# Kernel optimization log

Hardware: AMD Instinct MI355X
Metric: run time of the kernel (lower is better)

The kernel has to match this reference:

```python
import jax, jax.numpy as jnp
import numpy as np

B, S, D, E, L = 4, 384, 300, 50, 2
HD = D // L  # head_dim = 150


def _linear_params(k, fin, fout):
    bnd = 1.0 / np.sqrt(fin)
    kw, kb = jax.random.split(k)
    W = jax.random.uniform(kw, (fout, fin), minval=-bnd, maxval=bnd, dtype=jnp.float32)
    b = jax.random.uniform(kb, (fout,), minval=-bnd, maxval=bnd, dtype=jnp.float32)
    return W, b


def setup_inputs() -> dict:
    key = jax.random.key(0)
    ks = jax.random.split(key, 6)
    W0, b0 = _linear_params(ks[0], D, HD)            # weight_list[0]: Linear(300, 150)
    W1, b1 = _linear_params(ks[1], D + HD, HD)       # weight_list[1]: Linear(450, 150)
    Wh, bh = _linear_params(ks[2], 2 * HD + E, E)    # Edgeupdate.W: Linear(350, 50)
    Wout, bout = _linear_params(ks[3], D, D)         # linear_output: Linear(300, 300)
    adj = jax.random.uniform(ks[4], (B, S, S, E), dtype=jnp.float32)
    gcn_inputs = jax.random.normal(ks[5], (B, S, D), dtype=jnp.float32)
    return dict(adj=adj, gcn_inputs=gcn_inputs, W0=W0, b0=b0, W1=W1, b1=b1,
                Wh=Wh, bh=bh, Wout=Wout, bout=bout)


def reference(adj, gcn_inputs, W0, b0, W1, b1, Wh, bh, Wout, bout):
    # Edgeupdate weight split: cat order is [edge(E), node1(HD), node2(HD)]
    Wh_e = Wh[:, :E]            # [E, E]
    Wh_1 = Wh[:, E:E + HD]      # [E, HD]
    Wh_2 = Wh[:, E + HD:]       # [E, HD]

    outputs = gcn_inputs        # [B, S, D]
    cache = [gcn_inputs]
    out_list = []
    for (Wl, bl) in ((W0, b0), (W1, b1)):
        e_dim = adj.shape[-1]
        # mean over edge channels of (adj_e @ outputs): einsum fuses the mean
        Ax = jnp.einsum('bike,bkd->bid', adj, outputs) / e_dim   # [B, S, din]
        # AxW = W_l(Ax) + W_l(outputs)  (same linear applied twice, bias twice)
        AxW = (Ax @ Wl.T + bl) + (outputs @ Wl.T + bl)           # [B, S, HD]
        gAxW = jax.nn.relu(AxW)
        # Edgeupdate highway: new_edge[b,i,j] = W([edge[b,i,j]; g[b,j]; g[b,i]]) + bh
        # (node1[b,i,j] = g[b,j], node2[b,i,j] = g[b,i] from the expand/permute)
        edge_part = adj @ Wh_e.T                                  # [B, S, S, E]
        n1 = gAxW @ Wh_1.T                                        # [B, S, E]
        n2 = gAxW @ Wh_2.T                                        # [B, S, E]
        adj = edge_part + n1[:, None, :, :] + n2[:, :, None, :] + bh
        cache.append(gAxW)
        outputs = jnp.concatenate(cache, axis=2)                  # growing concat
        out_list.append(gAxW)  # gcn_drop is identity in eval mode

    gcn_outputs = jnp.concatenate(out_list, axis=2) + gcn_inputs  # [B, S, D]
    return gcn_outputs @ Wout.T + bout
```

## Files before the change

kernel.cpp:

```cpp
#include <hip/hip_runtime.h>

constexpr int Bc  = 4;
constexpr int Sc  = 384;
constexpr int Dc  = 300;
constexpr int Ec  = 50;
constexpr int HDc = 150;
constexpr int WHC = 350;

typedef __attribute__((ext_vector_type(8))) short bf16x8;
typedef __attribute__((ext_vector_type(4))) float f32x4;

__device__ __forceinline__ short f2bf(float x) {
    union { float f; unsigned u; } v; v.f = x;
    unsigned r = (v.u + 0x7FFFu + ((v.u >> 16) & 1u)) >> 16;
    return (short)r;
}

__global__ void prep_kernel(const float* __restrict__ Wh,
                            const float* __restrict__ bh,
                            float* __restrict__ sm) {
    int t = threadIdx.x;
    if (t < Ec) {
        float s = 0.f;
        for (int e = 0; e < Ec; ++e) s += Wh[e*WHC + t];
        sm[t] = s;
    } else if (t >= 64 && t < 64 + HDc) {
        int h = t - 64;
        float s = 0.f;
        for (int e = 0; e < Ec; ++e) s += Wh[e*WHC + Ec + h];
        sm[t] = s;
    } else if (t >= 224 && t < 224 + HDc) {
        int h = t - 224;
        float s = 0.f;
        for (int e = 0; e < Ec; ++e) s += Wh[e*WHC + Ec + HDc + h];
        sm[t] = s;
    } else if (t == 384) {
        float s = 0.f;
        for (int e = 0; e < Ec; ++e) s += bh[e];
        sm[t] = s;
    }
}

__global__ __launch_bounds__(256)
void reduce_adj3(const float* __restrict__ adj, const float* __restrict__ sm,
                 float* __restrict__ A0, float* __restrict__ wadj) {
    __shared__ float tile[64 * 51];
    __shared__ float wec[64];
    int t = threadIdx.x;
    if (t < Ec) wec[t] = sm[t];

    long base = (long)blockIdx.x * 3200;
    const float4* p4 = (const float4*)(adj + base);
    float4 v0 = p4[t];
    float4 v1 = p4[t + 256];
    float4 v2 = p4[t + 512];
    float4 v3 = {0.f, 0.f, 0.f, 0.f};
    if (t < 32) v3 = p4[t + 768];

    auto scat = [&](int i, const float4& v) {
        const float* vp = (const float*)&v;
        #pragma unroll
        for (int j = 0; j < 4; ++j) {
            int e = 4 * i + j;
            tile[(e / 50) * 51 + (e % 50)] = vp[j];
        }
    };
    scat(t, v0);
    scat(t + 256, v1);
    scat(t + 512, v2);
    if (t < 32) scat(t + 768, v3);
    __syncthreads();

    int r = t >> 2, q = t & 3;
    int h0 = q * 13, h1 = (q == 3) ? 50 : h0 + 13;
    const float* row = tile + r * 51;
    float s = 0.f, w = 0.f;
    for (int i = h0; i < h1; ++i) { float v = row[i]; s += v; w += v * wec[i]; }
    s += __shfl_xor(s, 1); w += __shfl_xor(w, 1);
    s += __shfl_xor(s, 2); w += __shfl_xor(w, 2);
    if (q == 0) {
        int g = blockIdx.x * 64 + r;
        A0[g]   = s * (1.0f / Ec);
        wadj[g] = w;
    }
}

template<int BSRC, int A1M, int HASD, int HASB, int RELU>
__global__ __launch_bounds__(256)
void mgemm(const float* __restrict__ A, int lda, long sA,
           const float* __restrict__ Bw, int ldb, long sB,
           const float* __restrict__ W1a, const float* __restrict__ WoutP,
           const float* __restrict__ Dm, int ldd, long sD,
           const float* __restrict__ bias, float bscale,
           const float* __restrict__ s12, const float* __restrict__ sm,
           float* __restrict__ C, int ldc, long sC,
           int M, int N, int K)
{
    const int b = blockIdx.z;
    const float* Ap = A + (long)b * sA;
    const float* Bp = Bw + (long)b * sB;
    const float* Dp = Dm + (long)b * sD;
    float* Cp = C + (long)b * sC;

    __shared__ short As[32 * 72];
    __shared__ short Bs[32 * 72];

    const int tid  = threadIdx.x;
    const int wave = tid >> 6, lane = tid & 63;
    const int wm = wave & 1, wn = wave >> 1;
    const int lm = lane & 15, quad = lane >> 4;
    const int m0 = blockIdx.y * 32, n0 = blockIdx.x * 32;

    const int srow = tid >> 3;
    const int sk   = (tid & 7) * 8;
    const int nc   = tid & 31;
    const int kr   = tid >> 5;

    float sbh = 0.f; const float* s1p = nullptr; float s2v = 0.f;
    if constexpr (A1M) {
        sbh = sm[384];
        s1p = s12 + 2L * Sc * b;
        s2v = s1p[2 * (m0 + srow) + 1];
    }

    float ra[8], rb[8];

    auto stageA = [&](int k0) {
        int am = m0 + srow;
        int kb = k0 + sk;
        if constexpr (A1M) {
            float4 u = *(const float4*)(Ap + (long)am * lda + kb);
            float4 w = *(const float4*)(Ap + (long)am * lda + kb + 4);
            const float* up = (const float*)&u;
            const float* wp = (const float*)&w;
            #pragma unroll
            for (int j = 0; j < 4; ++j) {
                ra[j]     = (up[j] + s1p[2*(kb + j)]     + s2v + sbh) * (1.0f/Ec);
                ra[4 + j] = (wp[j] + s1p[2*(kb + 4 + j)] + s2v + sbh) * (1.0f/Ec);
            }
        } else {
            if (kb + 7 < K) {
                float4 u = *(const float4*)(Ap + (long)am * lda + kb);
                float4 w = *(const float4*)(Ap + (long)am * lda + kb + 4);
                ra[0]=u.x; ra[1]=u.y; ra[2]=u.z; ra[3]=u.w;
                ra[4]=w.x; ra[5]=w.y; ra[6]=w.z; ra[7]=w.w;
            } else {
                #pragma unroll
                for (int j = 0; j < 8; ++j) {
                    int k = kb + j;
                    ra[j] = (k < K) ? Ap[(long)am * lda + k] : 0.f;
                }
            }
        }
    };

    auto stageB = [&](int k0) {
        if constexpr (BSRC == 0) {
            int n = n0 + nc;
            bool nok = n < N;
            #pragma unroll
            for (int p = 0; p < 8; ++p) {
                int k = k0 + kr + p * 8;
                rb[p] = nok ? Bp[(long)k * ldb + n] : 0.f;
            }
        } else {
            int nr = n0 + srow;
            bool nok = nr < N;
            const float* wp = Bp; int ld = ldb; int nn = nr;
            if constexpr (BSRC == 2) {
                if (nr < 150)      { wp = Bp;    ld = 300; nn = nr; }
                else if (nr < 300) { wp = W1a;   ld = 450; nn = nr - 150; }
                else               { wp = WoutP; ld = 300; nn = nr - 300; }
            }
            #pragma unroll
            for (int p = 0; p < 4; ++p) {
                int k = k0 + sk + 2 * p;
                if (nok && k + 1 < K) {
                    float2 v = *(const float2*)(wp + (long)nn * ld + k);
                    rb[2*p] = v.x; rb[2*p + 1] = v.y;
                } else {
                    rb[2*p]     = (nok && k < K)     ? wp[(long)nn * ld + k]     : 0.f;
                    rb[2*p + 1] = (nok && k + 1 < K) ? wp[(long)nn * ld + k + 1] : 0.f;
                }
            }
        }
    };

    auto stash = [&]() {
        #pragma unroll
        for (int j = 0; j < 8; ++j) As[srow * 72 + sk + j] = f2bf(ra[j]);
        if constexpr (BSRC == 0) {
            #pragma unroll
            for (int p = 0; p < 8; ++p) Bs[nc * 72 + kr + p * 8] = f2bf(rb[p]);
        } else {
            #pragma unroll
            for (int j = 0; j < 8; ++j) Bs[srow * 72 + sk + j] = f2bf(rb[j]);
        }
    };

    f32x4 acc = {0.f, 0.f, 0.f, 0.f};

    stageA(0); stageB(0);
    for (int k0 = 0; k0 < K; k0 += 64) {
        __syncthreads();
        stash();
        __syncthreads();
        if (k0 + 64 < K) { stageA(k0 + 64); stageB(k0 + 64); }
        {
            bf16x8 a0 = *(const bf16x8*)(As + (wm*16 + lm) * 72 + quad * 8);
            bf16x8 b0 = *(const bf16x8*)(Bs + (wn*16 + lm) * 72 + quad * 8);
            acc = __builtin_amdgcn_mfma_f32_16x16x32_bf16(a0, b0, acc, 0, 0, 0);
            bf16x8 a1 = *(const bf16x8*)(As + (wm*16 + lm) * 72 + 32 + quad * 8);
            bf16x8 b1 = *(const bf16x8*)(Bs + (wn*16 + lm) * 72 + 32 + quad * 8);
            acc = __builtin_amdgcn_mfma_f32_16x16x32_bf16(a1, b1, acc, 0, 0, 0);
        }
    }

    int cn = n0 + wn * 16 + lm;
    if (cn < N) {
        #pragma unroll
        for (int r = 0; r < 4; ++r) {
            int cm = m0 + wm * 16 + quad * 4 + r;
            if (cm < M) {
                float v = acc[r];
                if constexpr (HASD) v += Dp[(long)cm * ldd + cn];
                if constexpr (HASB) v += bscale * bias[cn];
                if constexpr (RELU) v = fmaxf(v, 0.f);
                Cp[(long)cm * ldc + cn] = v;
            }
        }
    }
}

__global__ __launch_bounds__(256)
void s12k(const float* __restrict__ G, const float* __restrict__ sm,
          float* __restrict__ s12) {
    int wave = threadIdx.x >> 6, lane = threadIdx.x & 63;
    int g = blockIdx.x * 4 + wave;
    const float* gp = G + (long)g * Dc;
    float a = 0.f, c = 0.f;
    #pragma unroll
    for (int h0 = 0; h0 < HDc; h0 += 64) {
        int h = h0 + lane;
        if (h < HDc) { float v = gp[h]; a += v * sm[64 + h]; c += v * sm[224 + h]; }
    }
    #pragma unroll
    for (int off = 32; off; off >>= 1) {
        a += __shfl_down(a, off);
        c += __shfl_down(c, off);
    }
    if (lane == 0) { s12[2*g] = a; s12[2*g + 1] = c; }
}

extern "C" void kernel_launch(void* const* d_in, const int* in_sizes, int n_in,
                              void* d_out, int out_size, void* d_ws, size_t ws_size,
                              hipStream_t stream) {
    const float* adj  = (const float*)d_in[0];
    const float* X    = (const float*)d_in[1];
    const float* W0   = (const float*)d_in[2];
    const float* b0   = (const float*)d_in[3];
    const float* W1   = (const float*)d_in[4];
    const float* b1   = (const float*)d_in[5];
    const float* Wh   = (const float*)d_in[6];
    const float* bh   = (const float*)d_in[7];
    const float* Wout = (const float*)d_in[8];
    const float* bout = (const float*)d_in[9];
    float* out = (float*)d_out;

    float* ws   = (float*)d_ws;
    float* sm   = ws;
    float* A0   = sm + 512;
    float* wadj = A0 + Bc * Sc * Sc;
    float* R    = wadj + Bc * Sc * Sc;
    float* Gbuf = R + (long)Bc * Sc * 600;
    float* s12  = Gbuf + (long)Bc * Sc * Dc;

    const int MT = Bc * Sc;
    const long AS = (long)Sc * Sc;
    const long RS = (long)Sc * 600;
    const long GS = (long)Sc * Dc;

    prep_kernel<<<1, 512, 0, stream>>>(Wh, bh, sm);

    reduce_adj3<<<(Bc*Sc*Sc) / 64, 256, 0, stream>>>(adj, sm, A0, wadj);

    mgemm<2,0,0,0,0><<<dim3(19, 48, 1), 256, 0, stream>>>(
        X, Dc, 0, W0, 300, 0, W1, Wout,
        nullptr, 0, 0, nullptr, 0.f, nullptr, nullptr,
        R, 600, 0, MT, 600, Dc);

    mgemm<0,0,1,1,1><<<dim3(5, 12, Bc), 256, 0, stream>>>(
        A0, Sc, AS, R, 600, RS, nullptr, nullptr,
        R, 600, RS, b0, 2.0f, nullptr, nullptr,
        Gbuf, Dc, GS, Sc, HDc, Sc);

    s12k<<<MT / 4, 256, 0, stream>>>(Gbuf, sm, s12);

    mgemm<1,0,1,0,0><<<dim3(5, 48, 1), 256, 0, stream>>>(
        Gbuf, Dc, 0, W1 + Dc, Dc + HDc, 0, nullptr, nullptr,
        R + HDc, 600, 0, nullptr, 0.f, nullptr, nullptr,
        R + HDc, 600, 0, MT, HDc, HDc);

    mgemm<0,1,1,1,1><<<dim3(5, 12, Bc), 256, 0, stream>>>(
        wadj, Sc, AS, R + HDc, 600, RS, nullptr, nullptr,
        R + HDc, 600, RS, b1, 2.0f, s12, sm,
        Gbuf + HDc, Dc, GS, Sc, HDc, Sc);

    mgemm<1,0,1,1,0><<<dim3(10, 48, 1), 256, 0, stream>>>(
        Gbuf, Dc, 0, Wout, Dc, 0, nullptr, nullptr,
        R + 2*HDc, 600, 0, bout, 1.0f, nullptr, nullptr,
        out, Dc, 0, MT, Dc, Dc);
}
```

Measured before the change: 242.9 us.

## Fuse all stages into one cooperative persistent kernel with grid syncs

```diff
diff --git a/kernel.cpp b/kernel.cpp
--- a/kernel.cpp
+++ b/kernel.cpp
@@ -1,4 +1,7 @@
 #include <hip/hip_runtime.h>
+#include <hip/hip_cooperative_groups.h>
+
+namespace cg = cooperative_groups;
 
 constexpr int Bc  = 4;
 constexpr int Sc  = 384;
@@ -6,6 +9,7 @@
 constexpr int Ec  = 50;
 constexpr int HDc = 150;
 constexpr int WHC = 350;
+constexpr int MT  = Bc * Sc;
 
 typedef __attribute__((ext_vector_type(8))) short bf16x8;
 typedef __attribute__((ext_vector_type(4))) float f32x4;
@@ -14,6 +18,334 @@
     union { float f; unsigned u; } v; v.f = x;
     unsigned r = (v.u + 0x7FFFu + ((v.u >> 16) & 1u)) >> 16;
     return (short)r;
+}
+
+
+__device__ __forceinline__ void reduce_unit(
+    float* tile, const float* wec,
+    const float* __restrict__ adj,
+    float* __restrict__ A0, float* __restrict__ wadj, int unit)
+{
+    int t = threadIdx.x;
+    __syncthreads();
+    long base = (long)unit * 3200;
+    const float4* p4 = (const float4*)(adj + base);
+    float4 v0 = p4[t];
+    float4 v1 = p4[t + 256];
+    float4 v2 = p4[t + 512];
+    float4 v3 = {0.f, 0.f, 0.f, 0.f};
+    if (t < 32) v3 = p4[t + 768];
+
+    auto scat = [&](int i, const float4& v) {
+        const float* vp = (const float*)&v;
+        #pragma unroll
+        for (int j = 0; j < 4; ++j) {
+            int e = 4 * i + j;
+            tile[(e / 50) * 51 + (e % 50)] = vp[j];
+        }
+    };
+    scat(t, v0);
+    scat(t + 256, v1);
+    scat(t + 512, v2);
+    if (t < 32) scat(t + 768, v3);
+    __syncthreads();
+
+    int r = t >> 2, q = t & 3;
+    int h0 = q * 13, h1 = (q == 3) ? 50 : h0 + 13;
+    const float* row = tile + r * 51;
+    float s = 0.f, w = 0.f;
+    for (int i = h0; i < h1; ++i) { float v = row[i]; s += v; w += v * wec[i]; }
+    s += __shfl_xor(s, 1); w += __shfl_xor(w, 1);
+    s += __shfl_xor(s, 2); w += __shfl_xor(w, 2);
+    if (q == 0) {
+        int g = unit * 64 + r;
+        A0[g]   = s * (1.0f / Ec);
+        wadj[g] = w;
+    }
+}
+
+__device__ __forceinline__ void s12_unit(const float* __restrict__ G,
+                                         const float* __restrict__ sm,
+                                         float* __restrict__ s12, int unit)
+{
+    int wave = threadIdx.x >> 6, lane = threadIdx.x & 63;
+    int g = unit * 4 + wave;
+    const float* gp = G + (long)g * Dc;
+    float a = 0.f, c = 0.f;
+    #pragma unroll
+    for (int h0 = 0; h0 < HDc; h0 += 64) {
+        int h = h0 + lane;
+        if (h < HDc) { float v = gp[h]; a += v * sm[64 + h]; c += v * sm[224 + h]; }
+    }
+    #pragma unroll
+    for (int off = 32; off; off >>= 1) {
+        a += __shfl_down(a, off);
+        c += __shfl_down(c, off);
+    }
+    if (lane == 0) { s12[2*g] = a; s12[2*g + 1] = c; }
+}
+
+template<int BSRC, int A1M, int HASD, int HASB, int RELU>
+__device__ __forceinline__ void mgemm_body(
+    short* As, short* Bs, int bx, int by, int b,
+    const float* __restrict__ A, int lda, long sA,
+    const float* __restrict__ Bw, int ldb, long sB,
+    const float* __restrict__ W1a, const float* __restrict__ WoutP,
+    const float* __restrict__ Dm, int ldd, long sD,
+    const float* __restrict__ bias, float bscale,
+    const float* __restrict__ s12, const float* __restrict__ sm,
+    float* __restrict__ C, int ldc, long sC,
+    int M, int N, int K)
+{
+    const float* Ap = A + (long)b * sA;
+    const float* Bp = Bw + (long)b * sB;
+    const float* Dp = Dm + (long)b * sD;
+    float* Cp = C + (long)b * sC;
+
+    const int tid  = threadIdx.x;
+    const int wave = tid >> 6, lane = tid & 63;
+    const int wm = wave & 1, wn = wave >> 1;
+    const int lm = lane & 15, quad = lane >> 4;
+    const int m0 = by * 32, n0 = bx * 32;
+
+    const int srow = tid >> 3;
+    const int sk   = (tid & 7) * 8;
+    const int nc   = tid & 31;
+    const int kr   = tid >> 5;
+
+    float sbh = 0.f; const float* s1p = nullptr; float s2v = 0.f;
+    if constexpr (A1M) {
+        sbh = sm[384];
+        s1p = s12 + 2L * Sc * b;
+        s2v = s1p[2 * (m0 + srow) + 1];
+    }
+
+    float ra[8], rb[8];
+
+    auto stageA = [&](int k0) {
+        int am = m0 + srow;
+        int kb = k0 + sk;
+        if constexpr (A1M) {
+            float4 u = *(const float4*)(Ap + (long)am * lda + kb);
+            float4 w = *(const float4*)(Ap + (long)am * lda + kb + 4);
+            const float* up = (const float*)&u;
+            const float* wp = (const float*)&w;
+            #pragma unroll
+            for (int j = 0; j < 4; ++j) {
+                ra[j]     = (up[j] + s1p[2*(kb + j)]     + s2v + sbh) * (1.0f/Ec);
+                ra[4 + j] = (wp[j] + s1p[2*(kb + 4 + j)] + s2v + sbh) * (1.0f/Ec);
+            }
+        } else {
+            if (kb + 7 < K) {
+                float4 u = *(const float4*)(Ap + (long)am * lda + kb);
+                float4 w = *(const float4*)(Ap + (long)am * lda + kb + 4);
+                ra[0]=u.x; ra[1]=u.y; ra[2]=u.z; ra[3]=u.w;
+                ra[4]=w.x; ra[5]=w.y; ra[6]=w.z; ra[7]=w.w;
+            } else {
+                #pragma unroll
+                for (int j = 0; j < 8; ++j) {
+                    int k = kb + j;
+                    ra[j] = (k < K) ? Ap[(long)am * lda + k] : 0.f;
+                }
+            }
+        }
+    };
+
+    auto stageB = [&](int k0) {
+        if constexpr (BSRC == 0) {
+            int n = n0 + nc;
+            bool nok = n < N;
+            #pragma unroll
+            for (int p = 0; p < 8; ++p) {
+                int k = k0 + kr + p * 8;
+                rb[p] = nok ? Bp[(long)k * ldb + n] : 0.f;
+            }
+        } else {
+            int nr = n0 + srow;
+            bool nok = nr < N;
+            const float* wp = Bp; int ld = ldb; int nn = nr;
+            if constexpr (BSRC == 2) {
+                if (nr < 150)      { wp = Bp;    ld = 300; nn = nr; }
+                else if (nr < 300) { wp = W1a;   ld = 450; nn = nr - 150; }
+                else               { wp = WoutP; ld = 300; nn = nr - 300; }
+            }
+            #pragma unroll
+            for (int p = 0; p < 4; ++p) {
+                int k = k0 + sk + 2 * p;
+                if (nok && k + 1 < K) {
+                    float2 v = *(const float2*)(wp + (long)nn * ld + k);
+                    rb[2*p] = v.x; rb[2*p + 1] = v.y;
+                } else {
+                    rb[2*p]     = (nok && k < K)     ? wp[(long)nn * ld + k]     : 0.f;
+                    rb[2*p + 1] = (nok && k + 1 < K) ? wp[(long)nn * ld + k + 1] : 0.f;
+                }
+            }
+        }
+    };
+
+    auto stash = [&]() {
+        #pragma unroll
+        for (int j = 0; j < 8; ++j) As[srow * 72 + sk + j] = f2bf(ra[j]);
+        if constexpr (BSRC == 0) {
+            #pragma unroll
+            for (int p = 0; p < 8; ++p) Bs[nc * 72 + kr + p * 8] = f2bf(rb[p]);
+        } else {
+            #pragma unroll
+            for (int j = 0; j < 8; ++j) Bs[srow * 72 + sk + j] = f2bf(rb[j]);
+        }
+    };
+
+    f32x4 acc = {0.f, 0.f, 0.f, 0.f};
+
+    stageA(0); stageB(0);
+    for (int k0 = 0; k0 < K; k0 += 64) {
+        __syncthreads();
+        stash();
+        __syncthreads();
+        if (k0 + 64 < K) { stageA(k0 + 64); stageB(k0 + 64); }
+        {
+            bf16x8 a0 = *(const bf16x8*)(As + (wm*16 + lm) * 72 + quad * 8);
+            bf16x8 b0 = *(const bf16x8*)(Bs + (wn*16 + lm) * 72 + quad * 8);
+            acc = __builtin_amdgcn_mfma_f32_16x16x32_bf16(a0, b0, acc, 0, 0, 0);
+            bf16x8 a1 = *(const bf16x8*)(As + (wm*16 + lm) * 72 + 32 + quad * 8);
+            bf16x8 b1 = *(const bf16x8*)(Bs + (wn*16 + lm) * 72 + 32 + quad * 8);
+            acc = __builtin_amdgcn_mfma_f32_16x16x32_bf16(a1, b1, acc, 0, 0, 0);
+        }
+    }
+
+    int cn = n0 + wn * 16 + lm;
+    if (cn < N) {
+        #pragma unroll
+        for (int r = 0; r < 4; ++r) {
+            int cm = m0 + wm * 16 + quad * 4 + r;
+            if (cm < M) {
+                float v = acc[r];
+                if constexpr (HASD) v += Dp[(long)cm * ldd + cn];
+                if constexpr (HASB) v += bscale * bias[cn];
+                if constexpr (RELU) v = fmaxf(v, 0.f);
+                Cp[(long)cm * ldc + cn] = v;
+            }
+        }
+    }
+}
+
+__global__ __launch_bounds__(256, 4)
+void mega(const float* __restrict__ adj, const float* __restrict__ X,
+          const float* __restrict__ W0, const float* __restrict__ b0,
+          const float* __restrict__ W1, const float* __restrict__ b1,
+          const float* __restrict__ Wh, const float* __restrict__ bh,
+          const float* __restrict__ Wout, const float* __restrict__ bout,
+          float* __restrict__ sm, float* __restrict__ A0,
+          float* __restrict__ wadj, float* __restrict__ R,
+          float* __restrict__ Gbuf, float* __restrict__ s12,
+          float* __restrict__ out)
+{
+    __shared__ float ldsf[64 * 51 + 64];
+    short* As   = (short*)ldsf;
+    short* Bs   = As + 32 * 72;
+    float* tile = ldsf;
+    float* wec  = ldsf + 64 * 51;
+
+    const int bid = blockIdx.x, nb = gridDim.x;
+    const int t = threadIdx.x;
+
+    if (t < Ec) {
+        float s = 0.f;
+        for (int e = 0; e < Ec; ++e) s += Wh[e * WHC + t];
+        wec[t] = s;
+    }
+    if (bid == 0) {
+        for (int u = t; u < 512; u += 256) {
+            if (u < Ec) {
+                float s = 0.f;
+                for (int e = 0; e < Ec; ++e) s += Wh[e*WHC + u];
+                sm[u] = s;
+            } else if (u >= 64 && u < 64 + HDc) {
+                int h = u - 64; float s = 0.f;
+                for (int e = 0; e < Ec; ++e) s += Wh[e*WHC + Ec + h];
+                sm[u] = s;
+            } else if (u >= 224 && u < 224 + HDc) {
+                int h = u - 224; float s = 0.f;
+                for (int e = 0; e < Ec; ++e) s += Wh[e*WHC + Ec + HDc + h];
+                sm[u] = s;
+            } else if (u == 384) {
+                float s = 0.f;
+                for (int e = 0; e < Ec; ++e) s += bh[e];
+                sm[u] = s;
+            }
+        }
+    }
+    __syncthreads();
+
+    const long AS = (long)Sc * Sc;
+    const long RS = (long)Sc * 600;
+    const long GS = (long)Sc * Dc;
+
+    cg::grid_group grid = cg::this_grid();
+
+    {
+        const int UR = (Bc * Sc * Sc) / 64;
+        const int UT = UR + 19 * 48;
+        for (int u = bid; u < UT; u += nb) {
+            if (u < UR) {
+                reduce_unit(tile, wec, adj, A0, wadj, u);
+            } else {
+                int v = u - UR;
+                mgemm_body<2,0,0,0,0>(As, Bs, v % 19, v / 19, 0,
+                    X, Dc, 0, W0, 300, 0, W1, Wout,
+                    nullptr, 0, 0, nullptr, 0.f, nullptr, nullptr,
+                    R, 600, 0, MT, 600, Dc);
+            }
+        }
+    }
+    grid.sync();
+
+    for (int u = bid; u < 5 * 12 * Bc; u += nb) {
+        mgemm_body<0,0,1,1,1>(As, Bs, u % 5, (u / 5) % 12, u / 60,
+            A0, Sc, AS, R, 600, RS, nullptr, nullptr,
+            R, 600, RS, b0, 2.0f, nullptr, nullptr,
+            Gbuf, Dc, GS, Sc, HDc, Sc);
+    }
+    grid.sync();
+
+    {
+        const int U1 = MT / 4;
+        const int U2 = U1 + 5 * 48;
+        const int U3 = U2 + 10 * 48;
+        for (int u = bid; u < U3; u += nb) {
+            if (u < U1) {
+                s12_unit(Gbuf, sm, s12, u);
+            } else if (u < U2) {
+                int v = u - U1;
+                mgemm_body<1,0,1,0,0>(As, Bs, v % 5, v / 5, 0,
+                    Gbuf, Dc, 0, W1 + Dc, Dc + HDc, 0, nullptr, nullptr,
+                    R + HDc, 600, 0, nullptr, 0.f, nullptr, nullptr,
+                    R + HDc, 600, 0, MT, HDc, HDc);
+            } else {
+                int v = u - U2;
+                mgemm_body<1,0,1,1,0>(As, Bs, v % 10, v / 10, 0,
+                    Gbuf, Dc, 0, Wout, Dc, 0, nullptr, nullptr,
+                    R + 2 * HDc, 600, 0, bout, 1.0f, nullptr, nullptr,
+                    out, Dc, 0, MT, Dc, HDc);
+            }
+        }
+    }
+    grid.sync();
+
+    for (int u = bid; u < 5 * 12 * Bc; u += nb) {
+        mgemm_body<0,1,1,1,1>(As, Bs, u % 5, (u / 5) % 12, u / 60,
+            wadj, Sc, AS, R + HDc, 600, RS, nullptr, nullptr,
+            R + HDc, 600, RS, b1, 2.0f, s12, sm,
+            Gbuf + HDc, Dc, GS, Sc, HDc, Sc);
+    }
+    grid.sync();
+
+    for (int u = bid; u < 10 * 48; u += nb) {
+        mgemm_body<1,0,1,0,0>(As, Bs, u % 10, u / 10, 0,
+            Gbuf + HDc, Dc, 0, Wout + HDc, Dc, 0, nullptr, nullptr,
+            out, Dc, 0, nullptr, 0.f, nullptr, nullptr,
+            out, Dc, 0, MT, Dc, HDc);
+    }
 }
 
 __global__ void prep_kernel(const float* __restrict__ Wh,
@@ -44,45 +376,11 @@
 __global__ __launch_bounds__(256)
 void reduce_adj3(const float* __restrict__ adj, const float* __restrict__ sm,
                  float* __restrict__ A0, float* __restrict__ wadj) {
-    __shared__ float tile[64 * 51];
-    __shared__ float wec[64];
-    int t = threadIdx.x;
-    if (t < Ec) wec[t] = sm[t];
-
-    long base = (long)blockIdx.x * 3200;
-    const float4* p4 = (const float4*)(adj + base);
-    float4 v0 = p4[t];
-    float4 v1 = p4[t + 256];
-    float4 v2 = p4[t + 512];
-    float4 v3 = {0.f, 0.f, 0.f, 0.f};
-    if (t < 32) v3 = p4[t + 768];
-
-    auto scat = [&](int i, const float4& v) {
-        const float* vp = (const float*)&v;
-        #pragma unroll
-        for (int j = 0; j < 4; ++j) {
-            int e = 4 * i + j;
-            tile[(e / 50) * 51 + (e % 50)] = vp[j];
-        }
-    };
-    scat(t, v0);
-    scat(t + 256, v1);
-    scat(t + 512, v2);
-    if (t < 32) scat(t + 768, v3);
-    __syncthreads();
-
-    int r = t >> 2, q = t & 3;
-    int h0 = q * 13, h1 = (q == 3) ? 50 : h0 + 13;
-    const float* row = tile + r * 51;
-    float s = 0.f, w = 0.f;
-    for (int i = h0; i < h1; ++i) { float v = row[i]; s += v; w += v * wec[i]; }
-    s += __shfl_xor(s, 1); w += __shfl_xor(w, 1);
-    s += __shfl_xor(s, 2); w += __shfl_xor(w, 2);
-    if (q == 0) {
-        int g = blockIdx.x * 64 + r;
-        A0[g]   = s * (1.0f / Ec);
-        wadj[g] = w;
-    }
+    __shared__ float lds[64 * 51 + 64];
+    float* tile = lds;
+    float* wec  = lds + 64 * 51;
+    if (threadIdx.x < Ec) wec[threadIdx.x] = sm[threadIdx.x];
+    reduce_unit(tile, wec, adj, A0, wadj, blockIdx.x);
 }
 
 template<int BSRC, int A1M, int HASD, int HASB, int RELU>
@@ -96,160 +394,18 @@
            float* __restrict__ C, int ldc, long sC,
            int M, int N, int K)
 {
-    const int b = blockIdx.z;
-    const float* Ap = A + (long)b * sA;
-    const float* Bp = Bw + (long)b * sB;
-    const float* Dp = Dm + (long)b * sD;
-    float* Cp = C + (long)b * sC;
-
     __shared__ short As[32 * 72];
     __shared__ short Bs[32 * 72];
-
-    const int tid  = threadIdx.x;
-    const int wave = tid >> 6, lane = tid & 63;
-    const int wm = wave & 1, wn = wave >> 1;
-    const int lm = lane & 15, quad = lane >> 4;
-    const int m0 = blockIdx.y * 32, n0 = blockIdx.x * 32;
-
-    const int srow = tid >> 3;
-    const int sk   = (tid & 7) * 8;
-    const int nc   = tid & 31;
-    const int kr   = tid >> 5;
-
-    float sbh = 0.f; const float* s1p = nullptr; float s2v = 0.f;
-    if constexpr (A1M) {
-        sbh = sm[384];
-        s1p = s12 + 2L * Sc * b;
-        s2v = s1p[2 * (m0 + srow) + 1];
-    }
-
-    float ra[8], rb[8];
-
-    auto stageA = [&](int k0) {
-        int am = m0 + srow;
-        int kb = k0 + sk;
-        if constexpr (A1M) {
-            float4 u = *(const float4*)(Ap + (long)am * lda + kb);
-            float4 w = *(const float4*)(Ap + (long)am * lda + kb + 4);
-            const float* up = (const float*)&u;
-            const float* wp = (const float*)&w;
-            #pragma unroll
-            for (int j = 0; j < 4; ++j) {
-                ra[j]     = (up[j] + s1p[2*(kb + j)]     + s2v + sbh) * (1.0f/Ec);
-                ra[4 + j] = (wp[j] + s1p[2*(kb + 4 + j)] + s2v + sbh) * (1.0f/Ec);
-            }
-        } else {
-            if (kb + 7 < K) {
-                float4 u = *(const float4*)(Ap + (long)am * lda + kb);
-                float4 w = *(const float4*)(Ap + (long)am * lda + kb + 4);
-                ra[0]=u.x; ra[1]=u.y; ra[2]=u.z; ra[3]=u.w;
-                ra[4]=w.x; ra[5]=w.y; ra[6]=w.z; ra[7]=w.w;
-            } else {
-                #pragma unroll
-                for (int j = 0; j < 8; ++j) {
-                    int k = kb + j;
-                    ra[j] = (k < K) ? Ap[(long)am * lda + k] : 0.f;
-                }
-            }
-        }
-    };
-
-    auto stageB = [&](int k0) {
-        if constexpr (BSRC == 0) {
-            int n = n0 + nc;
-            bool nok = n < N;
-            #pragma unroll
-            for (int p = 0; p < 8; ++p) {
-                int k = k0 + kr + p * 8;
-                rb[p] = nok ? Bp[(long)k * ldb + n] : 0.f;
-            }
-        } else {
-            int nr = n0 + srow;
-            bool nok = nr < N;
-            const float* wp = Bp; int ld = ldb; int nn = nr;
-            if constexpr (BSRC == 2) {
-                if (nr < 150)      { wp = Bp;    ld = 300; nn = nr; }
-                else if (nr < 300) { wp = W1a;   ld = 450; nn = nr - 150; }
-                else               { wp = WoutP; ld = 300; nn = nr - 300; }
-            }
-            #pragma unroll
-            for (int p = 0; p < 4; ++p) {
-                int k = k0 + sk + 2 * p;
-                if (nok && k + 1 < K) {
-                    float2 v = *(const float2*)(wp + (long)nn * ld + k);
-                    rb[2*p] = v.x; rb[2*p + 1] = v.y;
-                } else {
-                    rb[2*p]     = (nok && k < K)     ? wp[(long)nn * ld + k]     : 0.f;
-                    rb[2*p + 1] = (nok && k + 1 < K) ? wp[(long)nn * ld + k + 1] : 0.f;
-                }
-            }
-        }
-    };
-
-    auto stash = [&]() {
-        #pragma unroll
-        for (int j = 0; j < 8; ++j) As[srow * 72 + sk + j] = f2bf(ra[j]);
-        if constexpr (BSRC == 0) {
-            #pragma unroll
-            for (int p = 0; p < 8; ++p) Bs[nc * 72 + kr + p * 8] = f2bf(rb[p]);
-        } else {
-            #pragma unroll
-            for (int j = 0; j < 8; ++j) Bs[srow * 72 + sk + j] = f2bf(rb[j]);
-        }
-    };
-
-    f32x4 acc = {0.f, 0.f, 0.f, 0.f};
-
-    stageA(0); stageB(0);
-    for (int k0 = 0; k0 < K; k0 += 64) {
-        __syncthreads();
-        stash();
-        __syncthreads();
-        if (k0 + 64 < K) { stageA(k0 + 64); stageB(k0 + 64); }
-        {
-            bf16x8 a0 = *(const bf16x8*)(As + (wm*16 + lm) * 72 + quad * 8);
-            bf16x8 b0 = *(const bf16x8*)(Bs + (wn*16 + lm) * 72 + quad * 8);
-            acc = __builtin_amdgcn_mfma_f32_16x16x32_bf16(a0, b0, acc, 0, 0, 0);
-            bf16x8 a1 = *(const bf16x8*)(As + (wm*16 + lm) * 72 + 32 + quad * 8);
-            bf16x8 b1 = *(const bf16x8*)(Bs + (wn*16 + lm) * 72 + 32 + quad * 8);
-            acc = __builtin_amdgcn_mfma_f32_16x16x32_bf16(a1, b1, acc, 0, 0, 0);
-        }
-    }
-
-    int cn = n0 + wn * 16 + lm;
-    if (cn < N) {
-        #pragma unroll
-        for (int r = 0; r < 4; ++r) {
-            int cm = m0 + wm * 16 + quad * 4 + r;
-            if (cm < M) {
-                float v = acc[r];
-                if constexpr (HASD) v += Dp[(long)cm * ldd + cn];
-                if constexpr (HASB) v += bscale * bias[cn];
-                if constexpr (RELU) v = fmaxf(v, 0.f);
-                Cp[(long)cm * ldc + cn] = v;
-            }
-        }
-    }
+    mgemm_body<BSRC,A1M,HASD,HASB,RELU>(As, Bs,
+        blockIdx.x, blockIdx.y, blockIdx.z,
+        A, lda, sA, Bw, ldb, sB, W1a, WoutP, Dm, ldd, sD,
+        bias, bscale, s12, sm, C, ldc, sC, M, N, K);
 }
 
 __global__ __launch_bounds__(256)
 void s12k(const float* __restrict__ G, const float* __restrict__ sm,
           float* __restrict__ s12) {
-    int wave = threadIdx.x >> 6, lane = threadIdx.x & 63;
-    int g = blockIdx.x * 4 + wave;
-    const float* gp = G + (long)g * Dc;
-    float a = 0.f, c = 0.f;
-    #pragma unroll
-    for (int h0 = 0; h0 < HDc; h0 += 64) {
-        int h = h0 + lane;
-        if (h < HDc) { float v = gp[h]; a += v * sm[64 + h]; c += v * sm[224 + h]; }
-    }
-    #pragma unroll
-    for (int off = 32; off; off >>= 1) {
-        a += __shfl_down(a, off);
-        c += __shfl_down(c, off);
-    }
-    if (lane == 0) { s12[2*g] = a; s12[2*g + 1] = c; }
+    s12_unit(G, sm, s12, blockIdx.x);
 }
 
 extern "C" void kernel_launch(void* const* d_in, const int* in_sizes, int n_in,
@@ -275,39 +431,60 @@
     float* Gbuf = R + (long)Bc * Sc * 600;
     float* s12  = Gbuf + (long)Bc * Sc * Dc;
 
-    const int MT = Bc * Sc;
     const long AS = (long)Sc * Sc;
     const long RS = (long)Sc * 600;
     const long GS = (long)Sc * Dc;
 
-    prep_kernel<<<1, 512, 0, stream>>>(Wh, bh, sm);
-
-    reduce_adj3<<<(Bc*Sc*Sc) / 64, 256, 0, stream>>>(adj, sm, A0, wadj);
-
-    mgemm<2,0,0,0,0><<<dim3(19, 48, 1), 256, 0, stream>>>(
-        X, Dc, 0, W0, 300, 0, W1, Wout,
-        nullptr, 0, 0, nullptr, 0.f, nullptr, nullptr,
-        R, 600, 0, MT, 600, Dc);
-
-    mgemm<0,0,1,1,1><<<dim3(5, 12, Bc), 256, 0, stream>>>(
-        A0, Sc, AS, R, 600, RS, nullptr, nullptr,
-        R, 600, RS, b0, 2.0f, nullptr, nullptr,
-        Gbuf, Dc, GS, Sc, HDc, Sc);
-
-    s12k<<<MT / 4, 256, 0, stream>>>(Gbuf, sm, s12);
-
-    mgemm<1,0,1,0,0><<<dim3(5, 48, 1), 256, 0, stream>>>(
-        Gbuf, Dc, 0, W1 + Dc, Dc + HDc, 0, nullptr, nullptr,
-        R + HDc, 600, 0, nullptr, 0.f, nullptr, nullptr,
-        R + HDc, 600, 0, MT, HDc, HDc);
-
-    mgemm<0,1,1,1,1><<<dim3(5, 12, Bc), 256, 0, stream>>>(
-        wadj, Sc, AS, R + HDc, 600, RS, nullptr, nullptr,
-        R + HDc, 600, RS, b1, 2.0f, s12, sm,
-        Gbuf + HDc, Dc, GS, Sc, HDc, Sc);
-
-    mgemm<1,0,1,1,0><<<dim3(10, 48, 1), 256, 0, stream>>>(
-        Gbuf, Dc, 0, Wout, Dc, 0, nullptr, nullptr,
-        R + 2*HDc, 600, 0, bout, 1.0f, nullptr, nullptr,
-        out, Dc, 0, MT, Dc, Dc);
-}
+    static int grid_size = 0;
+    if (grid_size == 0) {
+        int nbm = 0;
+        if (hipOccupancyMaxActiveBlocksPerMultiprocessor(&nbm, mega, 256, 0) != hipSuccess || nbm < 1)
+            nbm = 2;
+        int ncu = 256;
+        hipDeviceProp_t prop;
+        int dev = 0;
+        (void)hipGetDevice(&dev);
+        if (hipGetDeviceProperties(&prop, dev) == hipSuccess && prop.multiProcessorCount > 0)
+            ncu = prop.multiProcessorCount;
+        long g = (long)nbm * ncu;
+        if (g > 1024) g = 1024;
+        if (g < 256)  g = 256;
+        grid_size = (int)g;
+    }
+
+    void* args[] = {
+        (void*)&adj, (void*)&X, (void*)&W0, (void*)&b0, (void*)&W1, (void*)&b1,
+        (void*)&Wh, (void*)&bh, (void*)&Wout, (void*)&bout,
+        (void*)&sm, (void*)&A0, (void*)&wadj, (void*)&R, (void*)&Gbuf,
+        (void*)&s12, (void*)&out
+    };
+
+    hipError_t err = hipLaunchCooperativeKernel(mega, dim3(grid_size), dim3(256),
+                                                args, 0u, stream);
+    if (err != hipSuccess) {
+        const int MT_ = MT;
+        prep_kernel<<<1, 512, 0, stream>>>(Wh, bh, sm);
+        reduce_adj3<<<(Bc*Sc*Sc) / 64, 256, 0, stream>>>(adj, sm, A0, wadj);
+        mgemm<2,0,0,0,0><<<dim3(19, 48, 1), 256, 0, stream>>>(
+            X, Dc, 0, W0, 300, 0, W1, Wout,
+            nullptr, 0, 0, nullptr, 0.f, nullptr, nullptr,
+            R, 600, 0, MT_, 600, Dc);
+        mgemm<0,0,1,1,1><<<dim3(5, 12, Bc), 256, 0, stream>>>(
+            A0, Sc, AS, R, 600, RS, nullptr, nullptr,
+            R, 600, RS, b0, 2.0f, nullptr, nullptr,
+            Gbuf, Dc, GS, Sc, HDc, Sc);
+        s12k<<<MT_ / 4, 256, 0, stream>>>(Gbuf, sm, s12);
+        mgemm<1,0,1,0,0><<<dim3(5, 48, 1), 256, 0, stream>>>(
+            Gbuf, Dc, 0, W1 + Dc, Dc + HDc, 0, nullptr, nullptr,
+            R + HDc, 600, 0, nullptr, 0.f, nullptr, nullptr,
+            R + HDc, 600, 0, MT_, HDc, HDc);
+        mgemm<0,1,1,1,1><<<dim3(5, 12, Bc), 256, 0, stream>>>(
+            wadj, Sc, AS, R + HDc, 600, RS, nullptr, nullptr,
+            R + HDc, 600, RS, b1, 2.0f, s12, sm,
+            Gbuf + HDc, Dc, GS, Sc, HDc, Sc);
+        mgemm<1,0,1,1,0><<<dim3(10, 48, 1), 256, 0, stream>>>(
+            Gbuf, Dc, 0, Wout, Dc, 0, nullptr, nullptr,
+            R + 2*HDc, 600, 0, bout, 1.0f, nullptr, nullptr,
+            out, Dc, 0, MT_, Dc, Dc);
+    }
+}
```

Result: slower. 492.0 us (+102.6%).

## Fuse independent kernels into combined launches and split output GEMM by K halves

Applied to the files above, without the earlier changes.

```diff
diff --git a/kernel.cpp b/kernel.cpp
--- a/kernel.cpp
+++ b/kernel.cpp
@@ -6,6 +6,7 @@
 constexpr int Ec  = 50;
 constexpr int HDc = 150;
 constexpr int WHC = 350;
+constexpr int MT  = Bc * Sc;
 
 typedef __attribute__((ext_vector_type(8))) short bf16x8;
 typedef __attribute__((ext_vector_type(4))) float f32x4;
@@ -16,100 +17,49 @@
     return (short)r;
 }
 
-__global__ void prep_kernel(const float* __restrict__ Wh,
-                            const float* __restrict__ bh,
-                            float* __restrict__ sm) {
-    int t = threadIdx.x;
-    if (t < Ec) {
-        float s = 0.f;
-        for (int e = 0; e < Ec; ++e) s += Wh[e*WHC + t];
-        sm[t] = s;
-    } else if (t >= 64 && t < 64 + HDc) {
-        int h = t - 64;
-        float s = 0.f;
-        for (int e = 0; e < Ec; ++e) s += Wh[e*WHC + Ec + h];
-        sm[t] = s;
-    } else if (t >= 224 && t < 224 + HDc) {
-        int h = t - 224;
-        float s = 0.f;
-        for (int e = 0; e < Ec; ++e) s += Wh[e*WHC + Ec + HDc + h];
-        sm[t] = s;
-    } else if (t == 384) {
-        float s = 0.f;
-        for (int e = 0; e < Ec; ++e) s += bh[e];
-        sm[t] = s;
-    }
-}
-
-__global__ __launch_bounds__(256)
-void reduce_adj3(const float* __restrict__ adj, const float* __restrict__ sm,
-                 float* __restrict__ A0, float* __restrict__ wadj) {
-    __shared__ float tile[64 * 51];
-    __shared__ float wec[64];
-    int t = threadIdx.x;
-    if (t < Ec) wec[t] = sm[t];
-
-    long base = (long)blockIdx.x * 3200;
-    const float4* p4 = (const float4*)(adj + base);
-    float4 v0 = p4[t];
-    float4 v1 = p4[t + 256];
-    float4 v2 = p4[t + 512];
-    float4 v3 = {0.f, 0.f, 0.f, 0.f};
-    if (t < 32) v3 = p4[t + 768];
-
-    auto scat = [&](int i, const float4& v) {
-        const float* vp = (const float*)&v;
-        #pragma unroll
-        for (int j = 0; j < 4; ++j) {
-            int e = 4 * i + j;
-            tile[(e / 50) * 51 + (e % 50)] = vp[j];
-        }
-    };
-    scat(t, v0);
-    scat(t + 256, v1);
-    scat(t + 512, v2);
-    if (t < 32) scat(t + 768, v3);
-    __syncthreads();
-
-    int r = t >> 2, q = t & 3;
-    int h0 = q * 13, h1 = (q == 3) ? 50 : h0 + 13;
-    const float* row = tile + r * 51;
-    float s = 0.f, w = 0.f;
-    for (int i = h0; i < h1; ++i) { float v = row[i]; s += v; w += v * wec[i]; }
-    s += __shfl_xor(s, 1); w += __shfl_xor(w, 1);
-    s += __shfl_xor(s, 2); w += __shfl_xor(w, 2);
-    if (q == 0) {
-        int g = blockIdx.x * 64 + r;
-        A0[g]   = s * (1.0f / Ec);
-        wadj[g] = w;
-    }
+__device__ __forceinline__ void s12_unit(const float* __restrict__ G,
+                                         const float* __restrict__ sm,
+                                         float* __restrict__ s12, int unit)
+{
+    int wave = threadIdx.x >> 6, lane = threadIdx.x & 63;
+    int g = unit * 4 + wave;
+    const float* gp = G + (long)g * Dc;
+    float a = 0.f, c = 0.f;
+    #pragma unroll
+    for (int h0 = 0; h0 < HDc; h0 += 64) {
+        int h = h0 + lane;
+        if (h < HDc) { float v = gp[h]; a += v * sm[64 + h]; c += v * sm[224 + h]; }
+    }
+    #pragma unroll
+    for (int off = 32; off; off >>= 1) {
+        a += __shfl_down(a, off);
+        c += __shfl_down(c, off);
+    }
+    if (lane == 0) { s12[2*g] = a; s12[2*g + 1] = c; }
 }
 
 template<int BSRC, int A1M, int HASD, int HASB, int RELU>
-__global__ __launch_bounds__(256)
-void mgemm(const float* __restrict__ A, int lda, long sA,
-           const float* __restrict__ Bw, int ldb, long sB,
-           const float* __restrict__ W1a, const float* __restrict__ WoutP,
-           const float* __restrict__ Dm, int ldd, long sD,
-           const float* __restrict__ bias, float bscale,
-           const float* __restrict__ s12, const float* __restrict__ sm,
-           float* __restrict__ C, int ldc, long sC,
-           int M, int N, int K)
-{
-    const int b = blockIdx.z;
+__device__ __forceinline__ void mgemm_body(
+    short* As, short* Bs, int bx, int by, int b,
+    const float* __restrict__ A, int lda, long sA,
+    const float* __restrict__ Bw, int ldb, long sB,
+    const float* __restrict__ W1a, const float* __restrict__ WoutP,
+    const float* __restrict__ Dm, int ldd, long sD,
+    const float* __restrict__ bias, float bscale,
+    const float* __restrict__ s12, const float* __restrict__ sm,
+    float* __restrict__ C, int ldc, long sC,
+    int M, int N, int K)
+{
     const float* Ap = A + (long)b * sA;
     const float* Bp = Bw + (long)b * sB;
     const float* Dp = Dm + (long)b * sD;
     float* Cp = C + (long)b * sC;
 
-    __shared__ short As[32 * 72];
-    __shared__ short Bs[32 * 72];
-
     const int tid  = threadIdx.x;
     const int wave = tid >> 6, lane = tid & 63;
     const int wm = wave & 1, wn = wave >> 1;
     const int lm = lane & 15, quad = lane >> 4;
-    const int m0 = blockIdx.y * 32, n0 = blockIdx.x * 32;
+    const int m0 = by * 32, n0 = bx * 32;
 
     const int srow = tid >> 3;
     const int sk   = (tid & 7) * 8;
@@ -232,24 +182,135 @@
     }
 }
 
+template<int BSRC, int A1M, int HASD, int HASB, int RELU>
 __global__ __launch_bounds__(256)
-void s12k(const float* __restrict__ G, const float* __restrict__ sm,
-          float* __restrict__ s12) {
-    int wave = threadIdx.x >> 6, lane = threadIdx.x & 63;
-    int g = blockIdx.x * 4 + wave;
-    const float* gp = G + (long)g * Dc;
-    float a = 0.f, c = 0.f;
-    #pragma unroll
-    for (int h0 = 0; h0 < HDc; h0 += 64) {
-        int h = h0 + lane;
-        if (h < HDc) { float v = gp[h]; a += v * sm[64 + h]; c += v * sm[224 + h]; }
-    }
-    #pragma unroll
-    for (int off = 32; off; off >>= 1) {
-        a += __shfl_down(a, off);
-        c += __shfl_down(c, off);
-    }
-    if (lane == 0) { s12[2*g] = a; s12[2*g + 1] = c; }
+void mgemm(const float* __restrict__ A, int lda, long sA,
+           const float* __restrict__ Bw, int ldb, long sB,
+           const float* __restrict__ W1a, const float* __restrict__ WoutP,
+           const float* __restrict__ Dm, int ldd, long sD,
+           const float* __restrict__ bias, float bscale,
+           const float* __restrict__ s12, const float* __restrict__ sm,
+           float* __restrict__ C, int ldc, long sC,
+           int M, int N, int K)
+{
+    __shared__ short As[32 * 72];
+    __shared__ short Bs[32 * 72];
+    mgemm_body<BSRC,A1M,HASD,HASB,RELU>(As, Bs,
+        blockIdx.x, blockIdx.y, blockIdx.z,
+        A, lda, sA, Bw, ldb, sB, W1a, WoutP, Dm, ldd, sD,
+        bias, bscale, s12, sm, C, ldc, sC, M, N, K);
+}
+
+__global__ __launch_bounds__(256)
+void fused1(const float* __restrict__ adj, const float* __restrict__ X,
+            const float* __restrict__ W0, const float* __restrict__ W1,
+            const float* __restrict__ Wout, const float* __restrict__ Wh,
+            const float* __restrict__ bh,
+            float* __restrict__ sm, float* __restrict__ A0,
+            float* __restrict__ wadj, float* __restrict__ R)
+{
+    __shared__ float lds[64 * 51 + 64];
+    const int bx = blockIdx.x, t = threadIdx.x;
+
+    if (bx < 912) {
+        short* As = (short*)lds;
+        short* Bs = As + 32 * 72;
+        mgemm_body<2,0,0,0,0>(As, Bs, bx % 19, bx / 19, 0,
+            X, Dc, 0, W0, 300, 0, W1, Wout,
+            nullptr, 0, 0, nullptr, 0.f, nullptr, nullptr,
+            R, 600, 0, MT, 600, Dc);
+    } else if (bx == 912) {
+        for (int u = t; u < 512; u += 256) {
+            if (u < Ec) {
+                float s = 0.f;
+                for (int e = 0; e < Ec; ++e) s += Wh[e*WHC + u];
+                sm[u] = s;
+            } else if (u >= 64 && u < 64 + HDc) {
+                int h = u - 64; float s = 0.f;
+                for (int e = 0; e < Ec; ++e) s += Wh[e*WHC + Ec + h];
+                sm[u] = s;
+            } else if (u >= 224 && u < 224 + HDc) {
+                int h = u - 224; float s = 0.f;
+                for (int e = 0; e < Ec; ++e) s += Wh[e*WHC + Ec + HDc + h];
+                sm[u] = s;
+            } else if (u == 384) {
+                float s = 0.f;
+                for (int e = 0; e < Ec; ++e) s += bh[e];
+                sm[u] = s;
+            }
+        }
+    } else {
+        const int unit = bx - 913;
+        float* tile = lds;
+        float* wec  = lds + 64 * 51;
+
+        long base = (long)unit * 3200;
+        const float4* p4 = (const float4*)(adj + base);
+        float4 v0 = p4[t];
+        float4 v1 = p4[t + 256];
+        float4 v2 = p4[t + 512];
+        float4 v3 = {0.f, 0.f, 0.f, 0.f};
+        if (t < 32) v3 = p4[t + 768];
+
+        if (t < Ec) {
+            float s = 0.f;
+            for (int e = 0; e < Ec; ++e) s += Wh[e * WHC + t];
+            wec[t] = s;
+        }
+
+        auto scat = [&](int i, const float4& v) {
+            const float* vp = (const float*)&v;
+            #pragma unroll
+            for (int j = 0; j < 4; ++j) {
+                int e = 4 * i + j;
+                tile[(e / 50) * 51 + (e % 50)] = vp[j];
+            }
+        };
+        scat(t, v0);
+        scat(t + 256, v1);
+        scat(t + 512, v2);
+        if (t < 32) scat(t + 768, v3);
+        __syncthreads();
+
+        int r = t >> 2, q = t & 3;
+        int h0 = q * 13, h1 = (q == 3) ? 50 : h0 + 13;
+        const float* row = tile + r * 51;
+        float s = 0.f, w = 0.f;
+        for (int i = h0; i < h1; ++i) { float v = row[i]; s += v; w += v * wec[i]; }
+        s += __shfl_xor(s, 1); w += __shfl_xor(w, 1);
+        s += __shfl_xor(s, 2); w += __shfl_xor(w, 2);
+        if (q == 0) {
+            int g = unit * 64 + r;
+            A0[g]   = s * (1.0f / Ec);
+            wadj[g] = w;
+        }
+    }
+}
+
+__global__ __launch_bounds__(256)
+void fused3(const float* __restrict__ Gbuf, const float* __restrict__ sm,
+            float* __restrict__ s12, const float* __restrict__ W1,
+            float* __restrict__ R, const float* __restrict__ Wout,
+            const float* __restrict__ bout, float* __restrict__ out)
+{
+    __shared__ short As[32 * 72];
+    __shared__ short Bs[32 * 72];
+    const int bx = blockIdx.x;
+
+    if (bx < 480) {
+        mgemm_body<1,0,1,1,0>(As, Bs, bx % 10, bx / 10, 0,
+            Gbuf, Dc, 0, Wout, Dc, 0, nullptr, nullptr,
+            R + 2 * HDc, 600, 0, bout, 1.0f, nullptr, nullptr,
+            out, Dc, 0, MT, Dc, HDc);
+    } else if (bx < 480 + 240) {
+        int v = bx - 480;
+        mgemm_body<1,0,1,0,0>(As, Bs, v % 5, v / 5, 0,
+            Gbuf, Dc, 0, W1 + Dc, Dc + HDc, 0, nullptr, nullptr,
+            R + HDc, 600, 0, nullptr, 0.f, nullptr, nullptr,
+            R + HDc, 600, 0, MT, HDc, HDc);
+    } else {
+        s12_unit(Gbuf, sm, s12, bx - 720);
+    }
 }
 
 extern "C" void kernel_launch(void* const* d_in, const int* in_sizes, int n_in,
@@ -275,39 +336,28 @@
     float* Gbuf = R + (long)Bc * Sc * 600;
     float* s12  = Gbuf + (long)Bc * Sc * Dc;
 
-    const int MT = Bc * Sc;
     const long AS = (long)Sc * Sc;
     const long RS = (long)Sc * 600;
     const long GS = (long)Sc * Dc;
 
-    prep_kernel<<<1, 512, 0, stream>>>(Wh, bh, sm);
-
-    reduce_adj3<<<(Bc*Sc*Sc) / 64, 256, 0, stream>>>(adj, sm, A0, wadj);
-
-    mgemm<2,0,0,0,0><<<dim3(19, 48, 1), 256, 0, stream>>>(
-        X, Dc, 0, W0, 300, 0, W1, Wout,
-        nullptr, 0, 0, nullptr, 0.f, nullptr, nullptr,
-        R, 600, 0, MT, 600, Dc);
+    fused1<<<912 + 1 + (Bc*Sc*Sc)/64, 256, 0, stream>>>(
+        adj, X, W0, W1, Wout, Wh, bh, sm, A0, wadj, R);
 
     mgemm<0,0,1,1,1><<<dim3(5, 12, Bc), 256, 0, stream>>>(
         A0, Sc, AS, R, 600, RS, nullptr, nullptr,
         R, 600, RS, b0, 2.0f, nullptr, nullptr,
         Gbuf, Dc, GS, Sc, HDc, Sc);
 
-    s12k<<<MT / 4, 256, 0, stream>>>(Gbuf, sm, s12);
-
-    mgemm<1,0,1,0,0><<<dim3(5, 48, 1), 256, 0, stream>>>(
-        Gbuf, Dc, 0, W1 + Dc, Dc + HDc, 0, nullptr, nullptr,
-        R + HDc, 600, 0, nullptr, 0.f, nullptr, nullptr,
-        R + HDc, 600, 0, MT, HDc, HDc);
+    fused3<<<480 + 240 + 384, 256, 0, stream>>>(
+        Gbuf, sm, s12, W1, R, Wout, bout, out);
 
     mgemm<0,1,1,1,1><<<dim3(5, 12, Bc), 256, 0, stream>>>(
         wadj, Sc, AS, R + HDc, 600, RS, nullptr, nullptr,
         R + HDc, 600, RS, b1, 2.0f, s12, sm,
         Gbuf + HDc, Dc, GS, Sc, HDc, Sc);
 
-    mgemm<1,0,1,1,0><<<dim3(10, 48, 1), 256, 0, stream>>>(
-        Gbuf, Dc, 0, Wout, Dc, 0, nullptr, nullptr,
-        R + 2*HDc, 600, 0, bout, 1.0f, nullptr, nullptr,
-        out, Dc, 0, MT, Dc, Dc);
-}
+    mgemm<1,0,1,0,0><<<dim3(10, 48, 1), 256, 0, stream>>>(
+        Gbuf + HDc, Dc, 0, Wout + HDc, Dc, 0, nullptr, nullptr,
+        out, Dc, 0, nullptr, 0.f, nullptr, nullptr,
+        out, Dc, 0, MT, Dc, HDc);
+}
```

Measured after the change: 227.2 us. 6.5% less time.
